# Kernel tuning notes

Hardware: AMD Instinct MI355X
Metric: run time of the kernel (lower is better)

Reference implementation:

```python
import jax, jax.numpy as jnp
import numpy as np

N = 50000      # nodes
E = 800000     # edges (before self loops)
G = 256        # graphs in batch
N_IN, NHID, HEADS, NOUT = 128, 64, 2, 768
ATT_SLOPE = 0.2   # GATv2 attention LeakyReLU slope (PyG default)
ACT_SLOPE = 0.01  # nn.LeakyReLU default slope


def setup_inputs() -> dict:
    key = jax.random.key(0)
    ks = jax.random.split(key, 20)
    def lin_w(k, fo, fi):
        return (jax.random.normal(k, (fo, fi), jnp.float32) / np.sqrt(fi)).astype(jnp.float32)
    x = jax.random.normal(ks[0], (N, N_IN), jnp.float32)
    edge_index = jax.random.randint(ks[1], (2, E), 0, N, dtype=jnp.int64)
    batch = jnp.sort(jax.random.randint(ks[2], (N,), 0, G, dtype=jnp.int64))
    HC = HEADS * NHID
    return {
        "x": x, "edge_index": edge_index, "batch": batch,
        # conv1: GATv2Conv(N_IN -> NHID, heads=HEADS)
        "w1_l": lin_w(ks[3], HC, N_IN), "b1_l": jnp.zeros((HC,), jnp.float32),
        "w1_r": lin_w(ks[4], HC, N_IN), "b1_r": jnp.zeros((HC,), jnp.float32),
        "att1": jax.random.normal(ks[5], (HEADS, NHID), jnp.float32) / np.sqrt(NHID),
        "bias1": jnp.zeros((HC,), jnp.float32),
        # conv2: GATv2Conv(HC -> NHID, heads=1)
        "w2_l": lin_w(ks[6], NHID, HC), "b2_l": jnp.zeros((NHID,), jnp.float32),
        "w2_r": lin_w(ks[7], NHID, HC), "b2_r": jnp.zeros((NHID,), jnp.float32),
        "att2": jax.random.normal(ks[8], (1, NHID), jnp.float32) / np.sqrt(NHID),
        "bias2": jnp.zeros((NHID,), jnp.float32),
        # MLP head
        "fc1_w": lin_w(ks[9], NHID, NHID), "fc1_b": jnp.zeros((NHID,), jnp.float32),
        "fc2_w": lin_w(ks[10], NOUT, NHID), "fc2_b": jnp.zeros((NOUT,), jnp.float32),
    }


def _leaky(v, slope):
    return jnp.where(v > 0, v, slope * v)


def gatv2_conv(x, src, dst, w_l, b_l, w_r, b_r, att, bias, heads, ch):
    n = x.shape[0]
    xl = (x @ w_l.T + b_l).reshape(n, heads, ch)   # source transform
    xr = (x @ w_r.T + b_r).reshape(n, heads, ch)   # target transform
    m = _leaky(xl[src] + xr[dst], ATT_SLOPE)       # [E, H, C]
    e = jnp.einsum('ehc,hc->eh', m, att)           # attention logits
    # segment softmax over incoming edges of each dst node (self loops guarantee non-empty)
    emax = jax.ops.segment_max(e, dst, num_segments=n)
    ex = jnp.exp(e - emax[dst])
    denom = jax.ops.segment_sum(ex, dst, num_segments=n)
    alpha = ex / denom[dst]
    out = jax.ops.segment_sum(xl[src] * alpha[:, :, None], dst, num_segments=n)
    return out.reshape(n, heads * ch) + bias


def reference(x, edge_index, batch, w1_l, b1_l, w1_r, b1_r, att1, bias1,
              w2_l, b2_l, w2_r, b2_r, att2, bias2, fc1_w, fc1_b, fc2_w, fc2_b):
    loops = jnp.arange(N, dtype=edge_index.dtype)
    src = jnp.concatenate([edge_index[0], loops])  # PyG adds self loops by default
    dst = jnp.concatenate([edge_index[1], loops])
    h = gatv2_conv(x, src, dst, w1_l, b1_l, w1_r, b1_r, att1, bias1, HEADS, NHID)
    h = _leaky(h, ACT_SLOPE)
    h = gatv2_conv(h, src, dst, w2_l, b2_l, w2_r, b2_r, att2, bias2, 1, NHID)
    h = _leaky(h, ACT_SLOPE)
    # global mean pool over graphs
    sums = jax.ops.segment_sum(h, batch, num_segments=G)
    cnt = jax.ops.segment_sum(jnp.ones((N,), h.dtype), batch, num_segments=G)
    pooled = sums / jnp.maximum(cnt, 1.0)[:, None]
    h = _leaky(pooled @ fc1_w.T + fc1_b, ACT_SLOPE)
    return h @ fc2_w.T + fc2_b
```

## Files before the change

### kernel.cpp

```cpp
#include <hip/hip_runtime.h>

#define ATT_SLOPE 0.2f
#define ACT_SLOPE 0.01f

typedef _Float16 half8  __attribute__((ext_vector_type(8)));
typedef _Float16 half2v __attribute__((ext_vector_type(2)));
typedef float    floatx4 __attribute__((ext_vector_type(4)));

#if defined(__has_builtin)
#if __has_builtin(__builtin_amdgcn_fdot2)
#define HAVE_FDOT2 1
#endif
#endif

__device__ __forceinline__ float lrelu(float v, float s) {
    return fmaxf(v, v * s);
}

__device__ __forceinline__ half2v lrelu2(half2v m) {
    half2v t = m * (_Float16)ATT_SLOPE;
    return __builtin_elementwise_max(m, t);
}

__device__ __forceinline__ float dot2(half2v a, half2v b, float c) {
#ifdef HAVE_FDOT2
    return __builtin_amdgcn_fdot2(a, b, c, false);
#else
    return c + (float)a[0] * (float)b[0] + (float)a[1] * (float)b[1];
#endif
}


__global__ __launch_bounds__(256) void k_count_rank(const int* __restrict__ ei, int E, int N,
                                                    int* __restrict__ deg,
                                                    int* __restrict__ rank) {
    int i = blockIdx.x * 256 + threadIdx.x;
    int total = E + N;
    if (i >= total) return;
    int dst = (i < E) ? ei[E + i] : (i - E);
    rank[i] = atomicAdd(&deg[dst], 1);
}

__global__ __launch_bounds__(256) void k_scan_block(const int* __restrict__ deg, int n,
                                                    int* __restrict__ rp1, int* __restrict__ bsum) {
    __shared__ int s[256];
    int tid = threadIdx.x;
    int i = blockIdx.x * 256 + tid;
    s[tid] = (i < n) ? deg[i] : 0;
    __syncthreads();
    for (int off = 1; off < 256; off <<= 1) {
        int t = (tid >= off) ? s[tid - off] : 0;
        __syncthreads();
        s[tid] += t;
        __syncthreads();
    }
    if (i < n) rp1[i] = s[tid];
    if (tid == 255) bsum[blockIdx.x] = s[255];
}

__global__ __launch_bounds__(256) void k_scan_add(int* __restrict__ rowptr,
                                                  const int* __restrict__ bsum, int n) {
    __shared__ int s[256];
    int tid = threadIdx.x, bid = blockIdx.x;
    s[tid] = (tid < bid) ? bsum[tid] : 0;
    __syncthreads();
    for (int off = 128; off > 0; off >>= 1) {
        if (tid < off) s[tid] += s[tid + off];
        __syncthreads();
    }
    int boff = s[0];
    int i = bid * 256 + tid;
    if (i < n) rowptr[i + 1] += boff;
    if (i == 0) rowptr[0] = 0;
}

__global__ __launch_bounds__(256) void k_scatter(const int* __restrict__ ei, int E, int N,
                                                 const int* __restrict__ rowptr,
                                                 const int* __restrict__ rank,
                                                 int* __restrict__ adj) {
    const int T = E + N;
    const int part = blockIdx.x & 7;
    const int rng = (N + 7) / 8;
    const int lo = part * rng, hi = min(N, lo + rng);
    const int nb = gridDim.x >> 3;
    for (int base = (int)(blockIdx.x >> 3) * 256; base < T; base += nb * 256) {
        int i = base + threadIdx.x;
        if (i >= T) continue;
        int dst = (i < E) ? ei[E + i] : (i - E);
        if (dst >= lo && dst < hi) {
            int src = (i < E) ? ei[i] : dst;
            adj[rowptr[dst] + rank[i]] = src;
        }
    }
}


__global__ __launch_bounds__(256) void k_encode_w(const float* __restrict__ w1l,
                                                  const float* __restrict__ w1r,
                                                  const float* __restrict__ w2l,
                                                  const float* __restrict__ w2r,
                                                  _Float16* __restrict__ W1h,
                                                  _Float16* __restrict__ W1lo,
                                                  _Float16* __restrict__ W2h,
                                                  _Float16* __restrict__ W2lo,
                                                  float* __restrict__ gsum, int gn,
                                                  int* __restrict__ deg, int n) {
    int i = blockIdx.x * 256 + threadIdx.x;
    if (i >= 49152 + gn + n) return;
    if (i >= 49152 + gn) {
        deg[i - 49152 - gn] = 0;
        return;
    }
    if (i >= 49152) {
        gsum[i - 49152] = 0.f;
        return;
    }
    float v;
    _Float16 *ph, *pl;
    int idx;
    if (i < 32768) {
        idx = i;
        v = (i < 16384) ? w1l[i] : w1r[i - 16384];
        ph = W1h; pl = W1lo;
    } else {
        int j = i - 32768;
        idx = j;
        v = (j < 8192) ? w2l[j] : w2r[j - 8192];
        ph = W2h; pl = W2lo;
    }
    _Float16 h = (_Float16)v;
    ph[idx] = h;
    pl[idx] = (_Float16)(v - (float)h);
}


template <int COUT, bool IN_F32>
__global__ __launch_bounds__(512) void gemm_mfma(const float* __restrict__ Af,
                                                 const _Float16* __restrict__ Ahi,
                                                 const _Float16* __restrict__ Alo, int n_rows,
                                                 const _Float16* __restrict__ Whi,
                                                 const _Float16* __restrict__ Wlo,
                                                 const float* __restrict__ B0,
                                                 const float* __restrict__ B1,
                                                 _Float16* __restrict__ out) {
    constexpr int NT = COUT / 16;
    constexpr int WS = 40;
    __shared__ _Float16 sWh[COUT][WS];
    __shared__ _Float16 sWl[COUT][WS];
    const int tid = threadIdx.x;
    const int lane = tid & 63, wv = tid >> 6;
    const int m = lane & 15, q = lane >> 4;
    const long row0 = ((long)blockIdx.x * 8 + wv) * 16;
    const bool active = row0 < n_rows;
    const long arow = row0 + m;

    floatx4 acc[NT] = {};
    for (int kk = 0; kk < 128; kk += 32) {
        __syncthreads();
        for (int t = tid; t < COUT * 4; t += 512) {
            int c = t >> 2, ch = t & 3;
            *(half8*)&sWh[c][ch * 8] = *(const half8*)&Whi[(size_t)c * 128 + kk + ch * 8];
            *(half8*)&sWl[c][ch * 8] = *(const half8*)&Wlo[(size_t)c * 128 + kk + ch * 8];
        }
        __syncthreads();
        if (active) {
            half8 ah, al;
            if constexpr (IN_F32) {
                float4 a0 = *(const float4*)&Af[(size_t)arow * 128 + kk + q * 8];
                float4 a1 = *(const float4*)&Af[(size_t)arow * 128 + kk + q * 8 + 4];
                float av[8] = {a0.x, a0.y, a0.z, a0.w, a1.x, a1.y, a1.z, a1.w};
                #pragma unroll
                for (int x = 0; x < 8; ++x) {
                    ah[x] = (_Float16)av[x];
                    al[x] = (_Float16)(av[x] - (float)ah[x]);
                }
            } else {
                ah = *(const half8*)&Ahi[(size_t)arow * 128 + kk + q * 8];
                al = *(const half8*)&Alo[(size_t)arow * 128 + kk + q * 8];
            }
            #pragma unroll
            for (int nt = 0; nt < NT; ++nt) {
                half8 bh = *(const half8*)&sWh[nt * 16 + m][q * 8];
                half8 bl = *(const half8*)&sWl[nt * 16 + m][q * 8];
                acc[nt] = __builtin_amdgcn_mfma_f32_16x16x32_f16(ah, bh, acc[nt], 0, 0, 0);
                acc[nt] = __builtin_amdgcn_mfma_f32_16x16x32_f16(al, bh, acc[nt], 0, 0, 0);
                acc[nt] = __builtin_amdgcn_mfma_f32_16x16x32_f16(ah, bl, acc[nt], 0, 0, 0);
            }
        }
    }
    if (active) {
        #pragma unroll
        for (int nt = 0; nt < NT; ++nt) {
            int col = nt * 16 + m;
            float b = (col < COUT / 2) ? B0[col] : B1[col - COUT / 2];
            #pragma unroll
            for (int r = 0; r < 4; ++r) {
                long grow = row0 + q * 4 + r;
                out[(size_t)grow * COUT + col] = (_Float16)(acc[nt][r] + b);
            }
        }
    }
}


__global__ __launch_bounds__(128) void conv1_fused(const _Float16* __restrict__ buf,
                                                   const int* __restrict__ rowptr,
                                                   const int* __restrict__ adj,
                                                   const float* __restrict__ att,
                                                   const float* __restrict__ bias,
                                                   _Float16* __restrict__ h1hi,
                                                   _Float16* __restrict__ h1lo, int n) {
    __shared__ _Float16 sxl[2][16][136];
    __shared__ _Float16 sxr[2][128];
    __shared__ float    sw[2][2][16];
    __shared__ _Float16 satt[128];
    const int tid = threadIdx.x, lane = tid & 63, wv = tid >> 6;
    satt[tid] = (_Float16)att[tid];
    __syncthreads();
    int node = blockIdx.x * 2 + wv;
    if (node >= n) return;

    const int jlane = lane & 15;
    const int grp = lane >> 4;
    const int chq = grp * 32;
    const int head = grp >> 1;
    const int wselg = lane >> 5;
    if (lane < 16)
        *(half8*)&sxr[wv][lane * 8] = *(const half8*)&buf[(size_t)node * 256 + 128 + lane * 8];
    asm volatile("s_waitcnt lgkmcnt(0)" ::: "memory");

    const int s = rowptr[node], e = rowptr[node + 1];
    float2 accA = {0.f, 0.f}, accB = {0.f, 0.f};
    float denA = 0.f, denB = 0.f;
    for (int c0 = s; c0 < e; c0 += 16) {
        const int cnt = min(16, e - c0);
        float sacc0 = 0.f, sacc1 = 0.f;
        if (jlane < cnt) {
            int src = adj[c0 + jlane];
            const _Float16* xlp = &buf[(size_t)src * 256 + chq];
            #pragma unroll
            for (int k = 0; k < 4; ++k) {
                half8 l = *(const half8*)&xlp[k * 8];
                half8 r = *(const half8*)&sxr[wv][chq + k * 8];
                half8 a = *(const half8*)&satt[chq + k * 8];
                *(half8*)&sxl[wv][jlane][chq + k * 8] = l;
                float* sp = (k & 1) ? &sacc1 : &sacc0;
                #pragma unroll
                for (int p = 0; p < 4; ++p) {
                    half2v lp = {l[2 * p], l[2 * p + 1]};
                    half2v rp = {r[2 * p], r[2 * p + 1]};
                    half2v ap = {a[2 * p], a[2 * p + 1]};
                    *sp = dot2(lrelu2(lp + rp), ap, *sp);
                }
            }
        }
        float sacc = sacc0 + sacc1;
        float efull = sacc + __shfl_xor(sacc, 16);
        if ((grp & 1) == 0 && jlane < cnt) sw[wv][head][jlane] = __expf(efull);
        asm volatile("s_waitcnt lgkmcnt(0)" ::: "memory");
        int j = 0;
        for (; j + 1 < cnt; j += 2) {
            float w0 = sw[wv][wselg][j], w1 = sw[wv][wselg][j + 1];
            half2v v0 = *(const half2v*)&sxl[wv][j][lane * 2];
            half2v v1 = *(const half2v*)&sxl[wv][j + 1][lane * 2];
            accA.x += w0 * (float)v0[0]; accA.y += w0 * (float)v0[1]; denA += w0;
            accB.x += w1 * (float)v1[0]; accB.y += w1 * (float)v1[1]; denB += w1;
        }
        if (j < cnt) {
            float w0 = sw[wv][wselg][j];
            half2v v0 = *(const half2v*)&sxl[wv][j][lane * 2];
            accA.x += w0 * (float)v0[0]; accA.y += w0 * (float)v0[1]; denA += w0;
        }
        asm volatile("s_waitcnt lgkmcnt(0)" ::: "memory");
    }
    float inv = 1.f / (denA + denB);
    float2 b = *(const float2*)&bias[lane * 2];
    float ox = lrelu((accA.x + accB.x) * inv + b.x, ACT_SLOPE);
    float oy = lrelu((accA.y + accB.y) * inv + b.y, ACT_SLOPE);
    half2v hv, lv;
    hv[0] = (_Float16)ox; lv[0] = (_Float16)(ox - (float)hv[0]);
    hv[1] = (_Float16)oy; lv[1] = (_Float16)(oy - (float)hv[1]);
    *(half2v*)&h1hi[(size_t)node * 128 + lane * 2] = hv;
    *(half2v*)&h1lo[(size_t)node * 128 + lane * 2] = lv;
}


__global__ __launch_bounds__(128) void conv2_fused(const _Float16* __restrict__ buf,
                                                   const int* __restrict__ rowptr,
                                                   const int* __restrict__ adj,
                                                   const float* __restrict__ att,
                                                   const float* __restrict__ bias,
                                                   const int* __restrict__ batch,
                                                   float* __restrict__ gsum, int n) {
    __shared__ _Float16 sxl[2][16][72];
    __shared__ _Float16 sxr[2][64];
    __shared__ float    sw[2][16];
    __shared__ _Float16 satt[64];
    const int tid = threadIdx.x, lane = tid & 63, wv = tid >> 6;
    if (tid < 64) satt[tid] = (_Float16)att[tid];
    __syncthreads();
    int node = blockIdx.x * 2 + wv;
    if (node >= n) return;

    const int jlane = lane & 15;
    const int grp = lane >> 4;
    const int chq = grp * 16;
    if (lane < 8)
        *(half8*)&sxr[wv][lane * 8] = *(const half8*)&buf[(size_t)node * 128 + 64 + lane * 8];
    asm volatile("s_waitcnt lgkmcnt(0)" ::: "memory");

    const int s = rowptr[node], e = rowptr[node + 1];
    float accA = 0.f, accB = 0.f, denA = 0.f, denB = 0.f;
    for (int c0 = s; c0 < e; c0 += 16) {
        const int cnt = min(16, e - c0);
        float sacc = 0.f;
        if (jlane < cnt) {
            int src = adj[c0 + jlane];
            const _Float16* xlp = &buf[(size_t)src * 128 + chq];
            #pragma unroll
            for (int k = 0; k < 2; ++k) {
                half8 l = *(const half8*)&xlp[k * 8];
                half8 r = *(const half8*)&sxr[wv][chq + k * 8];
                half8 a = *(const half8*)&satt[chq + k * 8];
                *(half8*)&sxl[wv][jlane][chq + k * 8] = l;
                #pragma unroll
                for (int p = 0; p < 4; ++p) {
                    half2v lp = {l[2 * p], l[2 * p + 1]};
                    half2v rp = {r[2 * p], r[2 * p + 1]};
                    half2v ap = {a[2 * p], a[2 * p + 1]};
                    sacc = dot2(lrelu2(lp + rp), ap, sacc);
                }
            }
        }
        float s1 = sacc + __shfl_xor(sacc, 16);
        float efull = s1 + __shfl_xor(s1, 32);
        if (grp == 0 && jlane < cnt) sw[wv][jlane] = __expf(efull);
        asm volatile("s_waitcnt lgkmcnt(0)" ::: "memory");
        int j = 0;
        for (; j + 1 < cnt; j += 2) {
            float w0 = sw[wv][j], w1 = sw[wv][j + 1];
            accA += w0 * (float)sxl[wv][j][lane];     denA += w0;
            accB += w1 * (float)sxl[wv][j + 1][lane]; denB += w1;
        }
        if (j < cnt) {
            float w0 = sw[wv][j];
            accA += w0 * (float)sxl[wv][j][lane];
            denA += w0;
        }
        asm volatile("s_waitcnt lgkmcnt(0)" ::: "memory");
    }
    float val = lrelu((accA + accB) / (denA + denB) + bias[lane], ACT_SLOPE);
    atomicAdd(&gsum[(size_t)batch[node] * 64 + lane], val);
}


__device__ __forceinline__ int lower_bound(const int* a, int n, int v) {
    int lo = 0, hi = n;
    while (lo < hi) { int mid = (lo + hi) >> 1; if (a[mid] < v) lo = mid + 1; else hi = mid; }
    return lo;
}

__global__ __launch_bounds__(256) void pool_mlp(const float* __restrict__ gsum,
                                                const int* __restrict__ batch,
                                                const float* __restrict__ fc1_w,
                                                const float* __restrict__ fc1_b,
                                                const float* __restrict__ fc2_w,
                                                const float* __restrict__ fc2_b,
                                                float* __restrict__ out, int n) {
    const int g = blockIdx.x;
    const int tid = threadIdx.x;
    __shared__ float pooled[64];
    __shared__ float hmid[64];

    int lo = lower_bound(batch, n, g);
    int hi = lower_bound(batch, n, g + 1);
    float inv = 1.f / (float)max(hi - lo, 1);

    if (tid < 64) pooled[tid] = gsum[(size_t)g * 64 + tid] * inv;
    __syncthreads();
    if (tid < 64) {
        float acc = fc1_b[tid];
        const float* w = &fc1_w[(size_t)tid * 64];
        #pragma unroll
        for (int k = 0; k < 64; ++k) acc += pooled[k] * w[k];
        hmid[tid] = lrelu(acc, ACT_SLOPE);
    }
    __syncthreads();
    for (int o = tid; o < 768; o += 256) {
        float acc = fc2_b[o];
        const float* w = &fc2_w[(size_t)o * 64];
        #pragma unroll
        for (int k = 0; k < 64; ++k) acc += hmid[k] * w[k];
        out[(size_t)g * 768 + o] = acc;
    }
}


extern "C" void kernel_launch(void* const* d_in, const int* in_sizes, int n_in,
                              void* d_out, int out_size, void* d_ws, size_t ws_size,
                              hipStream_t stream) {
    const float* x     = (const float*)d_in[0];
    const int*   ei    = (const int*)d_in[1];
    const int*   batch = (const int*)d_in[2];
    const float* w1_l  = (const float*)d_in[3];
    const float* b1_l  = (const float*)d_in[4];
    const float* w1_r  = (const float*)d_in[5];
    const float* b1_r  = (const float*)d_in[6];
    const float* att1  = (const float*)d_in[7];
    const float* bias1 = (const float*)d_in[8];
    const float* w2_l  = (const float*)d_in[9];
    const float* b2_l  = (const float*)d_in[10];
    const float* w2_r  = (const float*)d_in[11];
    const float* b2_r  = (const float*)d_in[12];
    const float* att2  = (const float*)d_in[13];
    const float* bias2 = (const float*)d_in[14];
    const float* fc1_w = (const float*)d_in[15];
    const float* fc1_b = (const float*)d_in[16];
    const float* fc2_w = (const float*)d_in[17];
    const float* fc2_b = (const float*)d_in[18];
    float* out = (float*)d_out;

    const int N = in_sizes[2];
    const int E = in_sizes[1] / 2;
    const int T = E + N;
    const int G = out_size / 768;

    char* ws = (char*)d_ws;
    size_t off = 0;
    auto alloc = [&](size_t bytes) -> void* {
        void* p = ws + off;
        off = (off + bytes + 255) & ~(size_t)255;
        return p;
    };
    int*      deg    = (int*)alloc((size_t)N * 4);
    int*      rowptr = (int*)alloc((size_t)(N + 1) * 4);
    int*      rank   = (int*)alloc((size_t)T * 4);
    int*      bsum   = (int*)alloc(1024);
    int*      adj    = (int*)alloc((size_t)T * 4);
    _Float16* h1hi   = (_Float16*)alloc((size_t)N * 128 * 2);
    _Float16* h1lo   = (_Float16*)alloc((size_t)N * 128 * 2);
    _Float16* W1h    = (_Float16*)alloc(32768 * 2);
    _Float16* W1lo   = (_Float16*)alloc(32768 * 2);
    _Float16* W2h    = (_Float16*)alloc(16384 * 2);
    _Float16* W2lo   = (_Float16*)alloc(16384 * 2);
    float*    gsum   = (float*)alloc((size_t)G * 64 * 4);
    _Float16* buf1   = (_Float16*)alloc((size_t)N * 256 * 2);
    _Float16* buf2 = buf1;

    const int nbN  = (N + 255) / 256;
    const int nbT  = (T + 255) / 256;
    const int mfmG = (N / 16 + 7) / 8;
    const int edgG = (N + 1) / 2;
    const int encG = (49152 + G * 64 + N + 255) / 256;

    k_encode_w<<<encG, 256, 0, stream>>>(w1_l, w1_r, w2_l, w2_r,
                                         W1h, W1lo, W2h, W2lo, gsum, G * 64, deg, N);

    k_count_rank<<<nbT, 256, 0, stream>>>(ei, E, N, deg, rank);
    k_scan_block<<<nbN, 256, 0, stream>>>(deg, N, rowptr + 1, bsum);
    k_scan_add<<<nbN, 256, 0, stream>>>(rowptr, bsum, N);
    k_scatter<<<2048, 256, 0, stream>>>(ei, E, N, rowptr, rank, adj);

    gemm_mfma<256, true><<<mfmG, 512, 0, stream>>>(x, nullptr, nullptr, N,
                                                   W1h, W1lo, b1_l, b1_r, buf1);
    conv1_fused<<<edgG, 128, 0, stream>>>(buf1, rowptr, adj, att1, bias1, h1hi, h1lo, N);

    gemm_mfma<128, false><<<mfmG, 512, 0, stream>>>(nullptr, h1hi, h1lo, N,
                                                    W2h, W2lo, b2_l, b2_r, buf2);
    conv2_fused<<<edgG, 128, 0, stream>>>(buf2, rowptr, adj, att2, bias2, batch, gsum, N);

    pool_mlp<<<G, 256, 0, stream>>>(gsum, batch, fc1_w, fc1_b, fc2_w, fc2_b, out, N);
}
```

Before: 298.1 us.

## Fuse CSR scatter into first GEMM launch and halve GEMM block size

Merges the adjacency scatter kernel into the conv1 GEMM kernel as extra blocks in a single grid, so the two independent jobs run concurrently in one launch. The scatter no longer partitions destinations into eight ranges across a grid-stride loop; each thread now handles one edge directly. GEMM blocks shrink from 512 to 256 threads (4 waves, 64 rows each), which doubles the grid and reloads the shared weight tiles twice as often per row. Dropping the dst-range partitioning may lose the write locality the old scatter was designed for.

```diff
diff --git a/kernel.cpp b/kernel.cpp
--- a/kernel.cpp
+++ b/kernel.cpp
@@ -72,26 +72,6 @@
     int i = bid * 256 + tid;
     if (i < n) rowptr[i + 1] += boff;
     if (i == 0) rowptr[0] = 0;
-}
-
-__global__ __launch_bounds__(256) void k_scatter(const int* __restrict__ ei, int E, int N,
-                                                 const int* __restrict__ rowptr,
-                                                 const int* __restrict__ rank,
-                                                 int* __restrict__ adj) {
-    const int T = E + N;
-    const int part = blockIdx.x & 7;
-    const int rng = (N + 7) / 8;
-    const int lo = part * rng, hi = min(N, lo + rng);
-    const int nb = gridDim.x >> 3;
-    for (int base = (int)(blockIdx.x >> 3) * 256; base < T; base += nb * 256) {
-        int i = base + threadIdx.x;
-        if (i >= T) continue;
-        int dst = (i < E) ? ei[E + i] : (i - E);
-        if (dst >= lo && dst < hi) {
-            int src = (i < E) ? ei[i] : dst;
-            adj[rowptr[dst] + rank[i]] = src;
-        }
-    }
 }
 
 
@@ -135,29 +115,27 @@
 
 
 template <int COUT, bool IN_F32>
-__global__ __launch_bounds__(512) void gemm_mfma(const float* __restrict__ Af,
-                                                 const _Float16* __restrict__ Ahi,
-                                                 const _Float16* __restrict__ Alo, int n_rows,
-                                                 const _Float16* __restrict__ Whi,
-                                                 const _Float16* __restrict__ Wlo,
-                                                 const float* __restrict__ B0,
-                                                 const float* __restrict__ B1,
-                                                 _Float16* __restrict__ out) {
+__device__ __forceinline__ void gemm_body(int bid, int tid,
+                                          _Float16 (*sWh)[40], _Float16 (*sWl)[40],
+                                          const float* __restrict__ Af,
+                                          const _Float16* __restrict__ Ahi,
+                                          const _Float16* __restrict__ Alo, int n_rows,
+                                          const _Float16* __restrict__ Whi,
+                                          const _Float16* __restrict__ Wlo,
+                                          const float* __restrict__ B0,
+                                          const float* __restrict__ B1,
+                                          _Float16* __restrict__ out) {
     constexpr int NT = COUT / 16;
-    constexpr int WS = 40;
-    __shared__ _Float16 sWh[COUT][WS];
-    __shared__ _Float16 sWl[COUT][WS];
-    const int tid = threadIdx.x;
     const int lane = tid & 63, wv = tid >> 6;
     const int m = lane & 15, q = lane >> 4;
-    const long row0 = ((long)blockIdx.x * 8 + wv) * 16;
+    const long row0 = ((long)bid * 4 + wv) * 16;
     const bool active = row0 < n_rows;
     const long arow = row0 + m;
 
     floatx4 acc[NT] = {};
     for (int kk = 0; kk < 128; kk += 32) {
         __syncthreads();
-        for (int t = tid; t < COUT * 4; t += 512) {
+        for (int t = tid; t < COUT * 4; t += 256) {
             int c = t >> 2, ch = t & 3;
             *(half8*)&sWh[c][ch * 8] = *(const half8*)&Whi[(size_t)c * 128 + kk + ch * 8];
             *(half8*)&sWl[c][ch * 8] = *(const half8*)&Wlo[(size_t)c * 128 + kk + ch * 8];
@@ -202,6 +180,48 @@
     }
 }
 
+__global__ __launch_bounds__(256) void k_gemm1_scatter(const float* __restrict__ x,
+                                                       const _Float16* __restrict__ W1h,
+                                                       const _Float16* __restrict__ W1lo,
+                                                       const float* __restrict__ B0,
+                                                       const float* __restrict__ B1,
+                                                       _Float16* __restrict__ buf1, int n_rows,
+                                                       const int* __restrict__ ei, int E,
+                                                       const int* __restrict__ rowptr,
+                                                       const int* __restrict__ rank,
+                                                       int* __restrict__ adj, int gB) {
+    __shared__ _Float16 sWh[256][40];
+    __shared__ _Float16 sWl[256][40];
+    const int bid = blockIdx.x, tid = threadIdx.x;
+    if (bid < gB) {
+        gemm_body<256, true>(bid, tid, sWh, sWl, x, nullptr, nullptr, n_rows,
+                             W1h, W1lo, B0, B1, buf1);
+    } else {
+        int i = (bid - gB) * 256 + tid;
+        int T = E + n_rows;
+        if (i < T) {
+            int dst = (i < E) ? ei[E + i] : (i - E);
+            int src = (i < E) ? ei[i] : dst;
+            adj[rowptr[dst] + rank[i]] = src;
+        }
+    }
+}
+
+template <int COUT, bool IN_F32>
+__global__ __launch_bounds__(256) void gemm_mfma(const float* __restrict__ Af,
+                                                 const _Float16* __restrict__ Ahi,
+                                                 const _Float16* __restrict__ Alo, int n_rows,
+                                                 const _Float16* __restrict__ Whi,
+                                                 const _Float16* __restrict__ Wlo,
+                                                 const float* __restrict__ B0,
+                                                 const float* __restrict__ B1,
+                                                 _Float16* __restrict__ out) {
+    __shared__ _Float16 sWh[COUT][40];
+    __shared__ _Float16 sWl[COUT][40];
+    gemm_body<COUT, IN_F32>(blockIdx.x, threadIdx.x, sWh, sWl, Af, Ahi, Alo, n_rows,
+                            Whi, Wlo, B0, B1, out);
+}
+
 
 __global__ __launch_bounds__(128) void conv1_fused(const _Float16* __restrict__ buf,
                                                    const int* __restrict__ rowptr,
@@ -449,7 +469,7 @@
 
     const int nbN  = (N + 255) / 256;
     const int nbT  = (T + 255) / 256;
-    const int mfmG = (N / 16 + 7) / 8;
+    const int mfmG = (N / 16 + 3) / 4;
     const int edgG = (N + 1) / 2;
     const int encG = (49152 + G * 64 + N + 255) / 256;
 
@@ -459,13 +479,13 @@
     k_count_rank<<<nbT, 256, 0, stream>>>(ei, E, N, deg, rank);
     k_scan_block<<<nbN, 256, 0, stream>>>(deg, N, rowptr + 1, bsum);
     k_scan_add<<<nbN, 256, 0, stream>>>(rowptr, bsum, N);
-    k_scatter<<<2048, 256, 0, stream>>>(ei, E, N, rowptr, rank, adj);
-
-    gemm_mfma<256, true><<<mfmG, 512, 0, stream>>>(x, nullptr, nullptr, N,
-                                                   W1h, W1lo, b1_l, b1_r, buf1);
+
+    k_gemm1_scatter<<<mfmG + nbT, 256, 0, stream>>>(x, W1h, W1lo, b1_l, b1_r, buf1, N,
+                                                    ei, E, rowptr, rank, adj, mfmG);
+
     conv1_fused<<<edgG, 128, 0, stream>>>(buf1, rowptr, adj, att1, bias1, h1hi, h1lo, N);
 
-    gemm_mfma<128, false><<<mfmG, 512, 0, stream>>>(nullptr, h1hi, h1lo, N,
+    gemm_mfma<128, false><<<mfmG, 256, 0, stream>>>(nullptr, h1hi, h1lo, N,
                                                     W2h, W2lo, b2_l, b2_r, buf2);
     conv2_fused<<<edgG, 128, 0, stream>>>(buf2, rowptr, adj, att2, bias2, batch, gsum, N);
 
```

Result: no change. 294.0 us (-1.4%).
